# Kernel optimization log

Hardware: AMD Instinct MI355X
Metric: run time of the kernel (lower is better)

Reference implementation:

```python
import jax, jax.numpy as jnp
import numpy as np

B, S, D, H, FF, P = 16, 200, 512, 8, 2048, 10
HD = D // H
EPS = 1e-5


def _pe2d(h, w, ch):
    # Faithful numpy port of PositionalEncoding2D (positional_encodings lib)
    channels = int(np.ceil(ch / 4) * 2)
    inv_freq = 1.0 / (10000.0 ** (np.arange(0, channels, 2, dtype=np.float32) / channels))
    sin_x = np.einsum('i,j->ij', np.arange(h, dtype=np.float32), inv_freq)
    sin_y = np.einsum('i,j->ij', np.arange(w, dtype=np.float32), inv_freq)
    emb_x = np.stack([np.sin(sin_x), np.cos(sin_x)], -1).reshape(h, channels)
    emb_y = np.stack([np.sin(sin_y), np.cos(sin_y)], -1).reshape(w, channels)
    emb = np.zeros((h, w, 2 * channels), dtype=np.float32)
    emb[:, :, :channels] = emb_x[:, None, :]
    emb[:, :, channels:2 * channels] = emb_y[None, :, :]
    return emb[:, :, :ch]


def _xavier(key, shape):
    fan_out, fan_in = shape
    lim = float(np.sqrt(6.0 / (fan_in + fan_out)))
    return jax.random.uniform(key, shape, minval=-lim, maxval=lim, dtype=jnp.float32)


def setup_inputs():
    key = jax.random.key(0)
    ks = jax.random.split(key, 8)
    x = jax.random.normal(ks[0], (B, S, D), dtype=jnp.float32)
    pos = jnp.asarray(_pe2d(S, S, P))  # (S, S, P) positional bias features
    Wkv = _xavier(ks[1], (2 * D, D)); bkv = jnp.zeros((2 * D,))
    Wo = _xavier(ks[2], (D, D)); bo = jnp.zeros((D,))
    Wpos = _xavier(ks[3], (1, P)); bpos = jnp.zeros((1,))
    W1 = _xavier(ks[4], (FF, D)); b1 = jnp.zeros((FF,))
    W2 = _xavier(ks[5], (D, FF)); b2 = jnp.zeros((D,))
    g1 = jnp.ones((D,)); beta1 = jnp.zeros((D,))
    g2 = jnp.ones((D,)); beta2 = jnp.zeros((D,))
    return {"x": x, "pos": pos, "Wkv": Wkv, "bkv": bkv, "Wo": Wo, "bo": bo,
            "Wpos": Wpos, "bpos": bpos, "W1": W1, "b1": b1, "W2": W2, "b2": b2,
            "g1": g1, "beta1": beta1, "g2": g2, "beta2": beta2}


def _layernorm(x, g, b):
    mu = jnp.mean(x, axis=-1, keepdims=True)
    var = jnp.mean(jnp.square(x - mu), axis=-1, keepdims=True)
    return (x - mu) * jax.lax.rsqrt(var + EPS) * g + b


def reference(x, pos, Wkv, bkv, Wo, bo, Wpos, bpos, W1, b1, W2, b2, g1, beta1, g2, beta2):
    # --- MultiheadAttention_KV (attn_type='kv') ---
    kv = x @ Wkv.T + bkv                                   # (B,S,2D)
    kv = kv.reshape(B, S, H, 2 * HD).transpose(0, 2, 1, 3)  # (B,H,S,2hd)
    k, v = kv[..., :HD], kv[..., HD:]
    attn = jnp.einsum('bhid,bhjd->bhij', k, k) / jnp.sqrt(jnp.float32(HD))
    # map_pos is linear: map_pos(attn[...,None] + pos) == attn*sum(w) + (pos@w + b)
    # -> same math as materializing the (B,H,S,S,P) tensor, but fused.
    pos_bias = pos @ Wpos[0] + bpos[0]                     # (S,S)
    scores = attn * jnp.sum(Wpos) + pos_bias[None, None]
    a = jax.nn.softmax(scores, axis=-1)
    vals = jnp.einsum('bhij,bhjd->bhid', a, v)             # (B,H,S,hd)
    vals = vals.transpose(0, 2, 1, 3).reshape(B, S, D)
    o = vals @ Wo.T + bo
    # --- residual + post-norm ---
    h = _layernorm(x + o, g1, beta1)
    # --- FFN ---
    ff = jax.nn.relu(h @ W1.T + b1) @ W2.T + b2
    return _layernorm(h + ff, g2, beta2)
```

## Files before the change

### kernel.cpp

```cpp
#include <hip/hip_runtime.h>
#include <hip/hip_bf16.h>

#define EPSV 1e-5f
static const int B_ = 16, S_ = 200, D_ = 512, H_ = 8, FF_ = 2048, P_ = 10, HD_ = 64;
static const int SP = 224;

typedef __bf16 bf16_t;
typedef __attribute__((ext_vector_type(8))) __bf16 bf16x8;
typedef __attribute__((ext_vector_type(4))) __bf16 bf16x4;
typedef __attribute__((ext_vector_type(4))) float f32x4;

__device__ __forceinline__ void gload16(const void* g, void* l) {
    __builtin_amdgcn_global_load_lds(
        (const __attribute__((address_space(1))) void*)g,
        (__attribute__((address_space(3))) void*)l, 16, 0, 0);
}

template <int BM, int BN, int WROWS, int WCOLS, int EPI>
__global__ __launch_bounds__(256) void mfma_gemm(
    const bf16_t* __restrict__ A,
    const bf16_t* __restrict__ Bw,
    bf16_t* __restrict__ Cb, long cBat, int ldc,
    const float* __restrict__ bias,
    bf16_t* __restrict__ kOut, bf16_t* __restrict__ vtOut,
    int M, int N, int K, int kcPerSplit)
{
    constexpr int MR = WROWS / 16, NR = WCOLS / 16;
    constexpr int NWC = BN / WCOLS;
    constexpr int NLOADS = BM / 32 + BN / 32;
    static_assert((4 / NWC) * WROWS == BM, "wave tiling must cover BM");
    static_assert(NWC * WCOLS == BN, "wave tiling must cover BN");
    static_assert(NLOADS == 6, "vmcnt literal below assumes 6 loads/stage");

    __shared__ bf16_t Asm[2][BM * 64];
    __shared__ bf16_t Bsm[2][BN * 64];

    const int wv = threadIdx.x >> 6;
    const int ln = threadIdx.x & 63;
    const int split = blockIdx.z;
    const int rowBase = blockIdx.y * BM;
    const int colBase = blockIdx.x * BN;
    const int wr = (wv / NWC) * WROWS;
    const int wc = (wv % NWC) * WCOLS;

    const int lr8 = ln >> 3;
    const int csw = ((ln & 7) ^ lr8) * 8;

    f32x4 acc[MR][NR] = {};

    const int kBeg = split * kcPerSplit;
    const int kEnd = kBeg + kcPerSplit;

    auto STAGE = [&](int k0, int buf) {
        #pragma unroll
        for (int i = 0; i < BM / 32; i++) {
            int row = i * 32 + wv * 8 + lr8;
            int gr = rowBase + row; gr = (gr < M) ? gr : (M - 1);
            gload16(A + (long)gr * K + k0 + csw, &Asm[buf][(i * 32 + wv * 8) * 64]);
        }
        #pragma unroll
        for (int i = 0; i < BN / 32; i++) {
            int col = i * 32 + wv * 8 + lr8;
            int gc = colBase + col; gc = (gc < N) ? gc : (N - 1);
            gload16(Bw + (long)gc * K + k0 + csw, &Bsm[buf][(i * 32 + wv * 8) * 64]);
        }
    };

    auto COMPUTE = [&](int buf) {
        #pragma unroll
        for (int kk = 0; kk < 2; kk++) {
            bf16x8 af[MR], bfr[NR];
            #pragma unroll
            for (int m = 0; m < MR; m++) {
                int r = wr + m * 16 + (ln & 15);
                int pc = (kk * 4 + (ln >> 4)) ^ (r & 7);
                af[m] = *reinterpret_cast<const bf16x8*>(&Asm[buf][r * 64 + pc * 8]);
            }
            #pragma unroll
            for (int n = 0; n < NR; n++) {
                int r = wc + n * 16 + (ln & 15);
                int pc = (kk * 4 + (ln >> 4)) ^ (r & 7);
                bfr[n] = *reinterpret_cast<const bf16x8*>(&Bsm[buf][r * 64 + pc * 8]);
            }
            #pragma unroll
            for (int m = 0; m < MR; m++)
                #pragma unroll
                for (int n = 0; n < NR; n++)
                    acc[m][n] = __builtin_amdgcn_mfma_f32_16x16x32_bf16(
                        af[m], bfr[n], acc[m][n], 0, 0, 0);
        }
    };

    STAGE(kBeg, 0);

    int t = 0;
    for (int k0 = kBeg; k0 < kEnd; k0 += 64, ++t) {
        const bool has_next = (k0 + 64 < kEnd);
        if (has_next) {
            STAGE(k0 + 64, (t + 1) & 1);
            asm volatile("s_waitcnt vmcnt(6)" ::: "memory");
        } else {
            asm volatile("s_waitcnt vmcnt(0)" ::: "memory");
        }
        __builtin_amdgcn_s_barrier();
        __builtin_amdgcn_sched_barrier(0);
        COMPUTE(t & 1);
        if (has_next) {
            __builtin_amdgcn_sched_barrier(0);
            __builtin_amdgcn_s_barrier();
        }
    }

    #pragma unroll
    for (int m = 0; m < MR; m++) {
        #pragma unroll
        for (int n = 0; n < NR; n++) {
            #pragma unroll
            for (int r = 0; r < 4; r++) {
                int row = rowBase + wr + m * 16 + (ln >> 4) * 4 + r;
                int col = colBase + wc + n * 16 + (ln & 15);
                if (row >= M || col >= N) continue;
                float v = acc[m][n][r];
                if constexpr (EPI == 3) {
                    v += bias[col];
                    int b = row / S_, s = row - b * S_;
                    int h = col >> 7, w = col & 127;
                    if (w < HD_)
                        kOut[((long)(b * H_ + h) * SP + s) * HD_ + w] = (bf16_t)v;
                    else
                        vtOut[((long)(b * H_ + h) * HD_ + (w - HD_)) * SP + s] = (bf16_t)v;
                } else if constexpr (EPI == 1) {
                    v += bias[col];
                    v = fmaxf(v, 0.f);
                    Cb[(long)row * ldc + col] = (bf16_t)v;
                } else {
                    Cb[(long)split * cBat + (long)row * ldc + col] = (bf16_t)v;
                }
            }
        }
    }
}

__global__ __launch_bounds__(256) void attn_fused(
    const bf16_t* __restrict__ Kb, const bf16_t* __restrict__ Vt,
    const float* __restrict__ G, const float* __restrict__ scalePtr,
    bf16_t* __restrict__ vals)
{
    __shared__ __align__(16) bf16_t Pl[4][16][232];

    const int bh = blockIdx.x;
    const int tile = blockIdx.y;
    const int wv = threadIdx.x >> 6;
    const int ln = threadIdx.x & 63;
    const int b = bh >> 3, h = bh & 7;
    const int rowBase = tile * 64 + wv * 16;

    const bf16_t* Kbh = Kb + (long)bh * SP * HD_;
    const bf16_t* Vbh = Vt + (long)bh * HD_ * SP;
    const float scale = scalePtr[0];

    const int lr = ln & 15;
    const int lk = (ln >> 4) * 8;

    f32x4 acc[14];
    #pragma unroll
    for (int n = 0; n < 14; n++) acc[n] = (f32x4){0.f, 0.f, 0.f, 0.f};

    int arow = rowBase + lr; arow = (arow < S_) ? arow : (S_ - 1);
    const bf16x8 a0 = *reinterpret_cast<const bf16x8*>(Kbh + (long)arow * HD_ + lk);
    const bf16x8 a1 = *reinterpret_cast<const bf16x8*>(Kbh + (long)arow * HD_ + 32 + lk);

    #pragma unroll
    for (int n = 0; n < 14; n++) {
        const bf16_t* bp = Kbh + (long)(n * 16 + lr) * HD_;
        bf16x8 b0 = *reinterpret_cast<const bf16x8*>(bp + lk);
        bf16x8 b1 = *reinterpret_cast<const bf16x8*>(bp + 32 + lk);
        acc[n] = __builtin_amdgcn_mfma_f32_16x16x32_bf16(a0, b0, acc[n], 0, 0, 0);
        acc[n] = __builtin_amdgcn_mfma_f32_16x16x32_bf16(a1, b1, acc[n], 0, 0, 0);
    }

    float Gc[14];
    #pragma unroll
    for (int n = 0; n < 14; n++) Gc[n] = G[n * 16 + lr];

    #pragma unroll
    for (int r = 0; r < 4; r++) {
        float m = -1e30f;
        #pragma unroll
        for (int n = 0; n < 14; n++) {
            float v = acc[n][r] * scale + Gc[n];
            acc[n][r] = v;
            m = fmaxf(m, v);
        }
        #pragma unroll
        for (int off = 1; off < 16; off <<= 1) m = fmaxf(m, __shfl_xor(m, off));
        float s = 0.f;
        #pragma unroll
        for (int n = 0; n < 14; n++) {
            float e = __expf(acc[n][r] - m);
            acc[n][r] = e;
            s += e;
        }
        #pragma unroll
        for (int off = 1; off < 16; off <<= 1) s += __shfl_xor(s, off);
        float inv = 1.f / s;
        #pragma unroll
        for (int n = 0; n < 14; n++) acc[n][r] *= inv;
    }

    #pragma unroll
    for (int n = 0; n < 14; n++)
        #pragma unroll
        for (int r = 0; r < 4; r++)
            Pl[wv][(ln >> 4) * 4 + r][n * 16 + lr] = (bf16_t)acc[n][r];

    f32x4 vacc[4] = {};
    #pragma unroll
    for (int kk = 0; kk < 7; kk++) {
        bf16x8 pa = *reinterpret_cast<const bf16x8*>(&Pl[wv][lr][kk * 32 + lk]);
        #pragma unroll
        for (int n = 0; n < 4; n++) {
            bf16x8 vb = *reinterpret_cast<const bf16x8*>(
                Vbh + (long)(n * 16 + lr) * SP + kk * 32 + lk);
            vacc[n] = __builtin_amdgcn_mfma_f32_16x16x32_bf16(pa, vb, vacc[n], 0, 0, 0);
        }
    }

    #pragma unroll
    for (int n = 0; n < 4; n++) {
        #pragma unroll
        for (int r = 0; r < 4; r++) {
            int row = rowBase + (ln >> 4) * 4 + r;
            if (row < S_)
                vals[((long)b * S_ + row) * D_ + h * HD_ + n * 16 + lr] =
                    (bf16_t)vacc[n][r];
        }
    }
}

__global__ __launch_bounds__(256) void prep_all(
    const float* __restrict__ x, const float* __restrict__ Wkv,
    const float* __restrict__ Wo, const float* __restrict__ W1,
    const float* __restrict__ W2, bf16_t* __restrict__ dst,
    float4* __restrict__ zeroP,
    const float* __restrict__ pos, const float* __restrict__ Wpos,
    float* __restrict__ G, float* __restrict__ scal)
{
    const int gid = blockIdx.x * blockDim.x + threadIdx.x;
    const int nthr = gridDim.x * blockDim.x;

    for (int i = gid; i < 1130496; i += nthr) {
        long e = (long)i * 4;
        const float* s; long off;
        if (e < 1638400)      { s = x;   off = e; }
        else if (e < 2162688) { s = Wkv; off = e - 1638400; }
        else if (e < 2424832) { s = Wo;  off = e - 2162688; }
        else if (e < 3473408) { s = W1;  off = e - 2424832; }
        else                  { s = W2;  off = e - 3473408; }
        float4 v = *reinterpret_cast<const float4*>(s + off);
        bf16x4 o = {(bf16_t)v.x, (bf16_t)v.y, (bf16_t)v.z, (bf16_t)v.w};
        *reinterpret_cast<bf16x4*>(dst + e) = o;
    }
    for (int i = gid; i < 458752; i += nthr)
        zeroP[i] = make_float4(0.f, 0.f, 0.f, 0.f);
    if (gid < SP) {
        float g = -1e30f;
        if (gid < S_) {
            g = 0.f;
            #pragma unroll
            for (int p = 6; p < 10; p++) g += pos[(long)gid * P_ + p] * Wpos[p];
        }
        G[gid] = g;
    }
    if (gid == 0) {
        float sw = 0.f;
        for (int p = 0; p < P_; p++) sw += Wpos[p];
        scal[0] = sw * 0.125f;
    }
}

template <int NPART, bool F32OUT>
__global__ __launch_bounds__(256) void add_ln_v(
    const bf16_t* __restrict__ a, const bf16_t* __restrict__ parts, long partStride,
    const float* __restrict__ bias,
    const float* __restrict__ g, const float* __restrict__ beta,
    float* __restrict__ outf, bf16_t* __restrict__ outb, int rows)
{
    int row = blockIdx.x * 4 + (threadIdx.x >> 6);
    int lane = threadIdx.x & 63;
    if (row >= rows) return;
    const int col = lane * 8;
    const long base = (long)row * D_ + col;

    bf16x8 a8 = *reinterpret_cast<const bf16x8*>(a + base);
    float4 b0 = *reinterpret_cast<const float4*>(bias + col);
    float4 b1 = *reinterpret_cast<const float4*>(bias + col + 4);
    const float bb[8] = {b0.x, b0.y, b0.z, b0.w, b1.x, b1.y, b1.z, b1.w};

    bf16x8 p8[NPART];
    #pragma unroll
    for (int p = 0; p < NPART; p++)
        p8[p] = *reinterpret_cast<const bf16x8*>(parts + (long)p * partStride + base);

    float v[8];
    float sum = 0.f;
    #pragma unroll
    for (int i = 0; i < 8; i++) {
        float t = (float)a8[i] + bb[i];
        #pragma unroll
        for (int p = 0; p < NPART; p++) t += (float)p8[p][i];
        v[i] = t;
        sum += t;
    }
    #pragma unroll
    for (int off = 32; off; off >>= 1) sum += __shfl_xor(sum, off);
    float mean = sum * (1.f / 512.f);
    float var = 0.f;
    #pragma unroll
    for (int i = 0; i < 8; i++) { float d = v[i] - mean; var += d * d; }
    #pragma unroll
    for (int off = 32; off; off >>= 1) var += __shfl_xor(var, off);
    float rstd = rsqrtf(var * (1.f / 512.f) + EPSV);

    float4 g0 = *reinterpret_cast<const float4*>(g + col);
    float4 g1v = *reinterpret_cast<const float4*>(g + col + 4);
    float4 e0 = *reinterpret_cast<const float4*>(beta + col);
    float4 e1 = *reinterpret_cast<const float4*>(beta + col + 4);
    const float gg[8] = {g0.x, g0.y, g0.z, g0.w, g1v.x, g1v.y, g1v.z, g1v.w};
    const float ee[8] = {e0.x, e0.y, e0.z, e0.w, e1.x, e1.y, e1.z, e1.w};

    if constexpr (F32OUT) {
        float4 o0, o1;
        o0.x = (v[0]-mean)*rstd*gg[0]+ee[0]; o0.y = (v[1]-mean)*rstd*gg[1]+ee[1];
        o0.z = (v[2]-mean)*rstd*gg[2]+ee[2]; o0.w = (v[3]-mean)*rstd*gg[3]+ee[3];
        o1.x = (v[4]-mean)*rstd*gg[4]+ee[4]; o1.y = (v[5]-mean)*rstd*gg[5]+ee[5];
        o1.z = (v[6]-mean)*rstd*gg[6]+ee[6]; o1.w = (v[7]-mean)*rstd*gg[7]+ee[7];
        *reinterpret_cast<float4*>(outf + base) = o0;
        *reinterpret_cast<float4*>(outf + base + 4) = o1;
    } else {
        bf16x8 o8;
        #pragma unroll
        for (int i = 0; i < 8; i++)
            o8[i] = (bf16_t)((v[i] - mean) * rstd * gg[i] + ee[i]);
        *reinterpret_cast<bf16x8*>(outb + base) = o8;
    }
}

extern "C" void kernel_launch(void* const* d_in, const int* in_sizes, int n_in,
                              void* d_out, int out_size, void* d_ws, size_t ws_size,
                              hipStream_t stream)
{
    const float* x    = (const float*)d_in[0];
    const float* pos  = (const float*)d_in[1];
    const float* Wkv  = (const float*)d_in[2];
    const float* bkv  = (const float*)d_in[3];
    const float* Wo   = (const float*)d_in[4];
    const float* bo   = (const float*)d_in[5];
    const float* Wpos = (const float*)d_in[6];
    const float* W1   = (const float*)d_in[8];
    const float* b1   = (const float*)d_in[9];
    const float* W2   = (const float*)d_in[10];
    const float* b2   = (const float*)d_in[11];
    const float* g1   = (const float*)d_in[12];
    const float* be1  = (const float*)d_in[13];
    const float* g2   = (const float*)d_in[14];
    const float* be2  = (const float*)d_in[15];
    float* out = (float*)d_out;

    char* w = (char*)d_ws;
    bf16_t* xb     = (bf16_t*)(w + 0);
    bf16_t* Wkvb   = (bf16_t*)(w + 3276800);
    bf16_t* Wob    = (bf16_t*)(w + 4325376);
    bf16_t* W1b    = (bf16_t*)(w + 4849664);
    bf16_t* W2b    = (bf16_t*)(w + 6946816);
    bf16_t* Kb     = (bf16_t*)(w + 9043968);
    bf16_t* Vt     = (bf16_t*)(w + 12713984);
    float*  G      = (float*)(w + 16384000);
    float*  scal   = (float*)(w + 16384896);
    bf16_t* vals   = (bf16_t*)(w + 16385024);
    bf16_t* hb     = (bf16_t*)(w + 19661824);
    bf16_t* obuf_b = (bf16_t*)(w + 22938624);
    bf16_t* tb     = (bf16_t*)(w + 29492224);
    bf16_t* fbuf_b = (bf16_t*)(w + 42599424);

    const int M = B_ * S_;
    const long PS = (long)M * D_;

    prep_all<<<2048, 256, 0, stream>>>(x, Wkv, Wo, W1, W2, xb, (float4*)Kb,
                                       pos, Wpos, G, scal);

    mfma_gemm<128, 64, 64, 32, 3><<<dim3(16, 25, 1), 256, 0, stream>>>(
        xb, Wkvb, nullptr, 0, 0, bkv, Kb, Vt, M, 2 * D_, D_, D_);

    attn_fused<<<dim3(128, 4, 1), 256, 0, stream>>>(Kb, Vt, G, scal, vals);

    mfma_gemm<128, 64, 64, 32, 5><<<dim3(8, 25, 2), 256, 0, stream>>>(
        vals, Wob, obuf_b, PS, D_, nullptr, nullptr, nullptr, M, D_, D_, 256);

    add_ln_v<2, false><<<(M + 3) / 4, 256, 0, stream>>>(
        xb, obuf_b, PS, bo, g1, be1, nullptr, hb, M);

    mfma_gemm<128, 64, 64, 32, 1><<<dim3(32, 25, 1), 256, 0, stream>>>(
        hb, W1b, tb, 0, FF_, b1, nullptr, nullptr, M, FF_, D_, D_);

    mfma_gemm<128, 64, 64, 32, 5><<<dim3(8, 25, 2), 256, 0, stream>>>(
        tb, W2b, fbuf_b, PS, D_, nullptr, nullptr, nullptr, M, D_, FF_, 1024);

    add_ln_v<2, true><<<(M + 3) / 4, 256, 0, stream>>>(
        hb, fbuf_b, PS, b2, g2, be2, out, nullptr, M);
}
```

Baseline: 109.3 us.

## Drop double-buffered LDS pipeline in GEMM and enlarge FFN1 tile to 128x128

The GEMM kernel loses its double-buffered prefetch: each K step now loads one LDS tile, syncs, computes, and syncs again, with no overlap between global loads and MFMA work. This halves LDS use per block, which may let more blocks share a CU. The FFN1 GEMM also moves to a 128x128 tile with 64x64 wave tiles, halving the grid and raising per-wave reuse. The cost is exposed load latency on every K step and fewer blocks for the FFN1 launch.

```diff
diff --git a/kernel.cpp b/kernel.cpp
--- a/kernel.cpp
+++ b/kernel.cpp
@@ -27,13 +27,11 @@
 {
     constexpr int MR = WROWS / 16, NR = WCOLS / 16;
     constexpr int NWC = BN / WCOLS;
-    constexpr int NLOADS = BM / 32 + BN / 32;
     static_assert((4 / NWC) * WROWS == BM, "wave tiling must cover BM");
     static_assert(NWC * WCOLS == BN, "wave tiling must cover BN");
-    static_assert(NLOADS == 6, "vmcnt literal below assumes 6 loads/stage");
-
-    __shared__ bf16_t Asm[2][BM * 64];
-    __shared__ bf16_t Bsm[2][BN * 64];
+
+    __shared__ bf16_t Asm[BM * 64];
+    __shared__ bf16_t Bsm[BN * 64];
 
     const int wv = threadIdx.x >> 6;
     const int ln = threadIdx.x & 63;
@@ -51,22 +49,21 @@
     const int kBeg = split * kcPerSplit;
     const int kEnd = kBeg + kcPerSplit;
 
-    auto STAGE = [&](int k0, int buf) {
+    for (int k0 = kBeg; k0 < kEnd; k0 += 64) {
         #pragma unroll
         for (int i = 0; i < BM / 32; i++) {
             int row = i * 32 + wv * 8 + lr8;
             int gr = rowBase + row; gr = (gr < M) ? gr : (M - 1);
-            gload16(A + (long)gr * K + k0 + csw, &Asm[buf][(i * 32 + wv * 8) * 64]);
+            gload16(A + (long)gr * K + k0 + csw, &Asm[(i * 32 + wv * 8) * 64]);
         }
         #pragma unroll
         for (int i = 0; i < BN / 32; i++) {
             int col = i * 32 + wv * 8 + lr8;
             int gc = colBase + col; gc = (gc < N) ? gc : (N - 1);
-            gload16(Bw + (long)gc * K + k0 + csw, &Bsm[buf][(i * 32 + wv * 8) * 64]);
-        }
-    };
-
-    auto COMPUTE = [&](int buf) {
+            gload16(Bw + (long)gc * K + k0 + csw, &Bsm[(i * 32 + wv * 8) * 64]);
+        }
+        __syncthreads();
+
         #pragma unroll
         for (int kk = 0; kk < 2; kk++) {
             bf16x8 af[MR], bfr[NR];
@@ -74,13 +71,13 @@
             for (int m = 0; m < MR; m++) {
                 int r = wr + m * 16 + (ln & 15);
                 int pc = (kk * 4 + (ln >> 4)) ^ (r & 7);
-                af[m] = *reinterpret_cast<const bf16x8*>(&Asm[buf][r * 64 + pc * 8]);
+                af[m] = *reinterpret_cast<const bf16x8*>(&Asm[r * 64 + pc * 8]);
             }
             #pragma unroll
             for (int n = 0; n < NR; n++) {
                 int r = wc + n * 16 + (ln & 15);
                 int pc = (kk * 4 + (ln >> 4)) ^ (r & 7);
-                bfr[n] = *reinterpret_cast<const bf16x8*>(&Bsm[buf][r * 64 + pc * 8]);
+                bfr[n] = *reinterpret_cast<const bf16x8*>(&Bsm[r * 64 + pc * 8]);
             }
             #pragma unroll
             for (int m = 0; m < MR; m++)
@@ -89,26 +86,7 @@
                     acc[m][n] = __builtin_amdgcn_mfma_f32_16x16x32_bf16(
                         af[m], bfr[n], acc[m][n], 0, 0, 0);
         }
-    };
-
-    STAGE(kBeg, 0);
-
-    int t = 0;
-    for (int k0 = kBeg; k0 < kEnd; k0 += 64, ++t) {
-        const bool has_next = (k0 + 64 < kEnd);
-        if (has_next) {
-            STAGE(k0 + 64, (t + 1) & 1);
-            asm volatile("s_waitcnt vmcnt(6)" ::: "memory");
-        } else {
-            asm volatile("s_waitcnt vmcnt(0)" ::: "memory");
-        }
-        __builtin_amdgcn_s_barrier();
-        __builtin_amdgcn_sched_barrier(0);
-        COMPUTE(t & 1);
-        if (has_next) {
-            __builtin_amdgcn_sched_barrier(0);
-            __builtin_amdgcn_s_barrier();
-        }
+        __syncthreads();
     }
 
     #pragma unroll
@@ -400,7 +378,7 @@
     add_ln_v<2, false><<<(M + 3) / 4, 256, 0, stream>>>(
         xb, obuf_b, PS, bo, g1, be1, nullptr, hb, M);
 
-    mfma_gemm<128, 64, 64, 32, 1><<<dim3(32, 25, 1), 256, 0, stream>>>(
+    mfma_gemm<128, 128, 64, 64, 1><<<dim3(16, 25, 1), 256, 0, stream>>>(
         hb, W1b, tb, 0, FF_, b1, nullptr, nullptr, M, FF_, D_, D_);
 
     mfma_gemm<128, 64, 64, 32, 5><<<dim3(8, 25, 2), 256, 0, stream>>>(
```

New measurement: 104.1 us. -4.8%, faster.
